# Performance work log

Hardware: AMD Instinct MI355X
Metric: run time of the kernel (lower is better)

The kernel has to match this reference:

```python
import jax, jax.numpy as jnp
import numpy as np

# graph / model constants (match init_kwargs and input_specs)
B, NPG, EPG, ML = 4, 10000, 32000, 128      # graphs, nodes/graph, edges/graph, latent
I_LAYERS, K_ITERS, J_HEADS = 3, 4, 6         # GNN layers, outer iters (n_iter+r_iter), I*n_iter
N, E, E2 = B * NPG, B * EPG, EPG // 2
ZETA = 1e-6
P_EXP = 1.852                                # Hazen-Williams exponent


def setup_inputs() -> dict:
    rng = np.random.default_rng(0)
    sndr_l, rcvr_l, r_l = [], [], []
    for b in range(B):
        off = b * NPG
        s = rng.integers(0, NPG, E2)
        t = rng.integers(0, NPG, E2)
        # per graph: first half forward edges, second half reversed (directionality trick)
        sndr_l.append(np.concatenate([s, t]) + off)
        rcvr_l.append(np.concatenate([t, s]) + off)
        rr = rng.uniform(0.1, 1.0, (E2, 1)).astype(np.float32)
        r_l.append(np.concatenate([rr, rr], 0))
    sndr = jnp.asarray(np.concatenate(sndr_l), dtype=jnp.int32)
    rcvr = jnp.asarray(np.concatenate(rcvr_l), dtype=jnp.int32)
    r = jnp.asarray(np.concatenate(r_l, 0))
    res = rng.random(N) < 0.01
    res[np.arange(B) * NPG] = True  # at least one reservoir per graph
    h_star = np.where(res, rng.uniform(50.0, 100.0, N), 0.0).astype(np.float32)
    d_star = rng.uniform(0.0, 0.1, N).astype(np.float32)
    x = jnp.asarray(np.stack([h_star, d_star], 1))
    ks = jax.random.split(jax.random.key(0), 9)
    def w(k, shape):
        return jax.random.normal(k, shape, jnp.float32) / np.sqrt(shape[-2])
    return dict(
        x=x, r=r,
        W_node_in=w(ks[0], (2, ML)), W_edge_in=w(ks[1], (2, ML)),
        Wf1=w(ks[2], (3 * ML, ML)), Wf2=w(ks[3], (ML, ML)), Wf3=w(ks[4], (ML, 1)),
        We1=w(ks[5], (I_LAYERS, 3 * ML, ML)), We2=w(ks[6], (I_LAYERS, ML, ML)),
        Wn1=w(ks[7], (I_LAYERS, 2 * ML, ML)), Wn2=w(ks[8], (I_LAYERS, ML, ML)),
        sndr=sndr, rcvr=rcvr)


def _compute_net_flows(h, r, sndr, rcvr):
    # invert Hazen-Williams: dh = r * sign(q) * |q|^1.852  =>  q = sign(dh)*(|dh|/r)^(1/1.852)
    dh = h[sndr] - h[rcvr]
    q = jnp.sign(dh) * ((jnp.abs(dh) + ZETA) / (r + ZETA)) ** (1.0 / P_EXP)
    d = jax.ops.segment_sum(q[:, 0], rcvr, num_segments=N)[:, None]
    return d, q


def _construct_heads(h_star, q, r, sndr, rcvr):
    # physics-informed head reconstruction: propagate heads from reservoirs along edges
    res = h_star != 0
    hl = r * jnp.sign(q) * jnp.abs(q) ** P_EXP  # head loss per edge
    h = h_star
    for _ in range(J_HEADS):
        cand = (h[sndr] - hl)[:, 0]
        agg = jax.ops.segment_max(cand, rcvr, num_segments=N)[:, None]
        agg = jnp.where(agg > -1e30, agg, h)  # nodes with no incoming edge keep value
        h = jnp.where(res, h_star, jnp.maximum(h, agg))
    return h


def _forward(x, r, W_node_in, W_edge_in, Wf1, Wf2, Wf3, We1, We2, Wn1, Wn2, sndr, rcvr):
    selu = jax.nn.selu
    h_star, d_star = x[:, 0:1], x[:, 1:2]
    d_hat, q_hat = _compute_net_flows(h_star, r, sndr, rcvr)
    q_tilde = q_hat
    h_tilde = h_star
    for _ in range(K_ITERS):
        # f_1: embed node/edge features
        g = selu(jnp.concatenate([d_hat, d_star], -1)) @ W_node_in    # [N, ML]
        z = selu(jnp.concatenate([q_tilde, q_hat], -1)) @ W_edge_in   # [E, ML]
        for i in range(I_LAYERS):
            # edge update MLP on (g_sndr, g_rcvr, z), then max-aggregate to nodes
            m = selu(jnp.concatenate([g[sndr], g[rcvr], z], -1))       # [E, 3ML]
            z = selu(m @ We1[i]) @ We2[i]
            agg = jax.ops.segment_max(z, rcvr, num_segments=N)
            agg = jnp.where(agg > -1e30, agg, 0.0)
            g = selu(selu(jnp.concatenate([g, agg], -1)) @ Wn1[i]) @ Wn2[i]
        # MLP lambda: flow residual
        lam_in = selu(jnp.concatenate([g[sndr], g[rcvr], z], -1))
        q_hat = q_hat + selu(selu(lam_in @ Wf1) @ Wf2) @ Wf3
        # enforce antisymmetric directionality: q(rev) = -q(fwd)
        q_in = q_hat.reshape(B, EPG, 1)[:, :E2]
        q_hat = jnp.concatenate([q_in, -q_in], axis=1).reshape(E, 1)
        # demand reconstruction (eq. 3): scatter-add flows into receivers
        d_hat = jax.ops.segment_sum(q_hat[:, 0], rcvr, num_segments=N)[:, None]
        # f_2: physics-informed head reconstruction + net flows (eq. 6-8)
        h_tilde = _construct_heads(h_star, q_hat, r, sndr, rcvr)
        d_tilde, q_tilde = _compute_net_flows(h_tilde, r, sndr, rcvr)
    return h_tilde


def reference(x, r, W_node_in, W_edge_in, Wf1, Wf2, Wf3, We1, We2, Wn1, Wn2, sndr, rcvr):
    return _forward(x, r, W_node_in, W_edge_in, Wf1, Wf2, Wf3, We1, We2, Wn1, Wn2, sndr, rcvr)
```

## Files before the change

### kernel.cpp

```cpp
#include <hip/hip_runtime.h>
#include <hip/hip_bf16.h>
#include <math.h>

#define NPGc  10000
#define EPGc  32000
#define MLc   128
#define NNc   40000
#define NEc   128000
#define E2c   16000
#define ZETAc 1e-6f
#define INVPc 0.53995680345572354f
#define PEXPc 1.852f
#define NSB   ((NNc + 255) / 256)

typedef __attribute__((ext_vector_type(8))) short short8;
typedef __attribute__((ext_vector_type(4))) float f32x4;

__device__ __forceinline__ float selu_f(float x) {
    float e = __expf(x) - 1.0f;
    return 1.0507009873554805f * (x > 0.0f ? x : 1.6732632423543772f * e);
}
__device__ __forceinline__ void splitt(float v, unsigned& hi, unsigned& lo) {
    unsigned u = __float_as_uint(v);
    hi = u >> 16;
    float rem = v - __uint_as_float(u & 0xffff0000u);
    __hip_bfloat16 l = __float2bfloat16(rem);
    lo = (unsigned short)*reinterpret_cast<short*>(&l);
}
__device__ __forceinline__ short bf16_rne(float v) {
    __hip_bfloat16 h = __float2bfloat16(v);
    return *reinterpret_cast<short*>(&h);
}
__device__ __forceinline__ float signf(float x) {
    return (x > 0.0f) ? 1.0f : (x < 0.0f ? -1.0f : 0.0f);
}
__device__ __forceinline__ int rfl(int v) { return __builtin_amdgcn_readfirstlane(v); }

__device__ __forceinline__ void load_lds16(const void* src, void* dst) {
    __builtin_amdgcn_global_load_lds(
        (const __attribute__((address_space(1))) unsigned*)src,
        (__attribute__((address_space(3))) unsigned*)dst, 16, 0, 0);
}

#define WCA (8 * 12 * 64)
#define WCB (8 * 4 * 64)
#define WCC (8 * 8 * 64)
#define WCTOT (3 * (WCA + WCB + WCC + WCB) + WCA + WCB)

__global__ void k_wconv_all(
    const float* __restrict__ We1, const float* __restrict__ We2,
    const float* __restrict__ Wn1, const float* __restrict__ Wn2,
    const float* __restrict__ Wf1, const float* __restrict__ Wf2,
    short* __restrict__ we1h, short* __restrict__ we2h,
    short* __restrict__ wn1h, short* __restrict__ wn2h,
    short* __restrict__ wf1h, short* __restrict__ wf2h) {
    int gid = blockIdx.x * 256 + threadIdx.x;
    if (gid >= WCTOT) return;
    const float* src; short* dst; int nkc; int lg;
    if (gid < 3 * WCA) {
        int L = gid / WCA; lg = gid - L * WCA;
        src = We1 + (size_t)L * 384 * 128; dst = we1h + (size_t)L * 128 * 384; nkc = 12;
    } else if (gid < 3 * WCA + 3 * WCB) {
        int g2 = gid - 3 * WCA; int L = g2 / WCB; lg = g2 - L * WCB;
        src = We2 + (size_t)L * 128 * 128; dst = we2h + (size_t)L * 128 * 128; nkc = 4;
    } else if (gid < 3 * WCA + 3 * WCB + 3 * WCC) {
        int g2 = gid - 3 * WCA - 3 * WCB; int L = g2 / WCC; lg = g2 - L * WCC;
        src = Wn1 + (size_t)L * 256 * 128; dst = wn1h + (size_t)L * 128 * 256; nkc = 8;
    } else if (gid < 3 * WCA + 3 * WCB + 3 * WCC + 3 * WCB) {
        int g2 = gid - 3 * WCA - 3 * WCB - 3 * WCC; int L = g2 / WCB; lg = g2 - L * WCB;
        src = Wn2 + (size_t)L * 128 * 128; dst = wn2h + (size_t)L * 128 * 128; nkc = 4;
    } else if (gid < 3 * WCA + 3 * WCB + 3 * WCC + 3 * WCB + WCA) {
        lg = gid - (3 * WCA + 3 * WCB + 3 * WCC + 3 * WCB);
        src = Wf1; dst = wf1h; nkc = 12;
    } else {
        lg = gid - (3 * WCA + 3 * WCB + 3 * WCC + 3 * WCB + WCA);
        src = Wf2; dst = wf2h; nkc = 4;
    }
    int lane = lg & 63;
    int frag = lg >> 6;
    int kc = frag % nkc;
    int ct = frag / nkc;
    int col = ct * 16 + (lane & 15);
    int kbase = kc * 32 + (lane >> 4) * 8;
    size_t o = (size_t)lg * 8;
#pragma unroll
    for (int j = 0; j < 8; j++)
        dst[o + j] = bf16_rne(src[(size_t)(kbase + j) * 128 + col]);
}

__global__ void k_zero_i(int* p, int n) {
    int i = blockIdx.x * 256 + threadIdx.x;
    if (i < n) p[i] = 0;
}
__global__ void k_count(const int* __restrict__ rcvr, int* __restrict__ deg) {
    int e = blockIdx.x * 256 + threadIdx.x;
    if (e < NEc) atomicAdd(&deg[rcvr[e]], 1);
}
__global__ void k_scan1(const int* __restrict__ deg, int* __restrict__ partial) {
    __shared__ int buf[256];
    int t = threadIdx.x;
    int i = blockIdx.x * 256 + t;
    buf[t] = (i < NNc) ? deg[i] : 0;
    __syncthreads();
    for (int off = 128; off > 0; off >>= 1) {
        if (t < off) buf[t] += buf[t + off];
        __syncthreads();
    }
    if (t == 0) partial[blockIdx.x] = buf[0];
}
__global__ void k_scan2(int* __restrict__ partial) {
    __shared__ int buf[256];
    int t = threadIdx.x;
    int v = (t < NSB) ? partial[t] : 0;
    buf[t] = v;
    __syncthreads();
    for (int off = 1; off < 256; off <<= 1) {
        int u = (t >= off) ? buf[t - off] : 0;
        __syncthreads();
        buf[t] += u;
        __syncthreads();
    }
    if (t < NSB) partial[t] = buf[t] - v;
}
__global__ void k_scan3(const int* __restrict__ deg, const int* __restrict__ partial,
                        int* __restrict__ rowstart, int* __restrict__ cursor) {
    __shared__ int buf[256];
    int t = threadIdx.x;
    int i = blockIdx.x * 256 + t;
    int v = (i < NNc) ? deg[i] : 0;
    buf[t] = v;
    __syncthreads();
    for (int off = 1; off < 256; off <<= 1) {
        int u = (t >= off) ? buf[t - off] : 0;
        __syncthreads();
        buf[t] += u;
        __syncthreads();
    }
    int excl = partial[blockIdx.x] + buf[t] - v;
    if (i < NNc) { rowstart[i] = excl; cursor[i] = excl; }
    if (i == NNc - 1) rowstart[NNc] = excl + v;
}
__global__ void k_scatter(const int* __restrict__ sndr, const int* __restrict__ rcvr,
                          int* __restrict__ cursor, int2* __restrict__ csr_se) {
    int e = blockIdx.x * 256 + threadIdx.x;
    if (e >= NEc) return;
    int rv = rcvr[e];
    int p = atomicAdd(&cursor[rv], 1);
    csr_se[p] = make_int2(sndr[e], e);
}

__global__ void k_qinit(const float* __restrict__ x, const float* __restrict__ r,
                        const int* __restrict__ sndr, const int* __restrict__ rcvr,
                        float* __restrict__ qh, float* __restrict__ qt) {
    int e = blockIdx.x * 256 + threadIdx.x;
    if (e >= NEc) return;
    float hv = x[2 * sndr[e]] - x[2 * rcvr[e]];
    float q = signf(hv) * __powf((fabsf(hv) + ZETAc) / (r[e] + ZETAc), INVPc);
    qh[e] = q; qt[e] = q;
}
__global__ void k_flows_q(const float* __restrict__ h, const float* __restrict__ r,
                          const int* __restrict__ sndr, const int* __restrict__ rcvr,
                          float* __restrict__ qt) {
    int e = blockIdx.x * 256 + threadIdx.x;
    if (e >= NEc) return;
    float hv = h[sndr[e]] - h[rcvr[e]];
    qt[e] = signf(hv) * __powf((fabsf(hv) + ZETAc) / (r[e] + ZETAc), INVPc);
}

__global__ __launch_bounds__(256) void k_node_in_f(
    const float* __restrict__ qh, const int* __restrict__ rowstart,
    const int2* __restrict__ csr_se, const float* __restrict__ x,
    const float* __restrict__ W ,
    unsigned* __restrict__ gh_u, unsigned* __restrict__ gl_u) {
    const int tid = threadIdx.x;
    const int lane = tid & 63;
    const int n = rfl(blockIdx.x * 4 + (tid >> 6));
    if (n >= NNc) return;
    int p0 = rfl(rowstart[n]), p1 = rfl(rowstart[n + 1]);
    float s = 0.0f;
    for (int p = p0 + lane; p < p1; p += 64) s += qh[csr_se[p].y];
#pragma unroll
    for (int off = 1; off < 64; off <<= 1) s += __shfl_xor(s, off, 64);
    float s0 = selu_f(s);
    float s1 = selu_f(x[2 * n + 1]);
    int c = lane * 2;
    float g0 = s0 * W[c]     + s1 * W[MLc + c];
    float g1 = s0 * W[c + 1] + s1 * W[MLc + c + 1];
    unsigned h0, l0, h1, l1;
    splitt(selu_f(g0), h0, l0);
    splitt(selu_f(g1), h1, l1);
    gh_u[(size_t)n * 64 + lane] = h0 | (h1 << 16);
    gl_u[(size_t)n * 64 + lane] = l0 | (l1 << 16);
}

__global__ __launch_bounds__(256) void k_head_iter(
    const float* __restrict__ x, const float* __restrict__ hin, int hstride,
    const float* __restrict__ hl, const int* __restrict__ rowstart,
    const int2* __restrict__ csr_se, float* __restrict__ hout) {
    int t = blockIdx.x * 256 + threadIdx.x;
    int n = t >> 2;
    int sub = t & 3;
    if (n >= NNc) return;
    float hv = hin[(size_t)n * hstride];
    float m = -3.0e38f;
    int p0 = rowstart[n], p1 = rowstart[n + 1];
    for (int p = p0 + sub; p < p1; p += 4) {
        int2 se = csr_se[p];
        m = fmaxf(m, hin[(size_t)se.x * hstride] - hl[se.y]);
    }
    m = fmaxf(m, __shfl_xor(m, 1, 64));
    m = fmaxf(m, __shfl_xor(m, 2, 64));
    if (sub == 0) {
        float a = (m > -1e30f) ? m : hv;
        float hstar = x[2 * n];
        hout[n] = (hstar != 0.0f) ? hstar : fmaxf(hv, a);
    }
}


__global__ __launch_bounds__(512) void k_edge_mlp_mfma(
    const unsigned* __restrict__ gh_u, const unsigned* __restrict__ gl_u,
    const unsigned* __restrict__ zh_u, const unsigned* __restrict__ zl_u,
    short* __restrict__ zoh_s, short* __restrict__ zol_s,
    const short* __restrict__ W1h, const short* __restrict__ W2h,
    const int* __restrict__ sndr, const int* __restrict__ rcvr,
    const float* __restrict__ qt, const float* __restrict__ qh,
    const float* __restrict__ Wei, int zmode) {
    __shared__ short smem[12288];
    const int tid = threadIdx.x;
    const int bi = blockIdx.x;
    const int x7 = bi & 7, jj = bi >> 3;
    const int e0 = ((x7 >> 1) * 1000 + (x7 & 1) * 500 + jj) * 32;
    const int lane = tid & 63, wave = tid >> 6;
    const int l15 = lane & 15, quad = lane >> 4;

    const int plane = wave & 1;
    const int srt = (wave >> 1) & 1;
    const int kc0 = wave >> 2;
    const int erow = e0 + srt * 16 + l15;
    const size_t bs = (size_t)sndr[erow] * 64 + quad * 4;
    const size_t br = (size_t)rcvr[erow] * 64 + quad * 4;
    const size_t bz = (size_t)erow * 64 + quad * 4;
    const unsigned* pg = plane ? gl_u : gh_u;
    const unsigned* pz = plane ? zl_u : zh_u;
    short* dbase = smem + plane * 6144 + srt * 512;
    const int nkc = zmode ? 8 : 12;

    short8 zvh, zvl;
    const int kzi = wave >> 1, rtz = wave & 1;
    if (zmode) {
        const int e = e0 + rtz * 16 + l15;
        const float sqt = selu_f(qt[e]), sqh = selu_f(qh[e]);
#pragma unroll
        for (int j = 0; j < 8; j++) {
            int c = kzi * 32 + quad * 8 + j;
            float z = sqt * Wei[c] + sqh * Wei[MLc + c];
            unsigned h, l;
            splitt(selu_f(z), h, l);
            zvh[j] = (short)h; zvl[j] = (short)l;
        }
    }

#pragma unroll
    for (int u = 0; u < 3; u++) {
        int kc = kc0 + 2 * u;
        int region = kc >> 2, kcl = kc & 3;
        const unsigned* src = (region == 0) ? (pg + bs + kcl * 16)
                                            : (pg + br + kcl * 16);
        load_lds16(src, dbase + kc * 1024);
    }
    __syncthreads();

    const int ct = wave;
    const int col = ct * 16 + l15;
    const short* abase = smem + lane * 8;

    f32x4 acc[2];
    acc[0] = (f32x4){0.f, 0.f, 0.f, 0.f};
    acc[1] = (f32x4){0.f, 0.f, 0.f, 0.f};
    __builtin_amdgcn_s_setprio(1);
#pragma unroll
    for (int kc = 0; kc < 6; kc++) {
        size_t wo = ((size_t)(ct * 12 + kc) * 64 + lane) * 8;
        short8 bh = *(const short8*)&W1h[wo];
#pragma unroll
        for (int rt = 0; rt < 2; rt++) {
            const short* ap = abase + (kc * 2 + rt) * 512;
            short8 ah = *(const short8*)ap;
            short8 al = *(const short8*)(ap + 6144);
            acc[rt] = __builtin_amdgcn_mfma_f32_16x16x32_bf16(ah, bh, acc[rt], 0, 0, 0);
            acc[rt] = __builtin_amdgcn_mfma_f32_16x16x32_bf16(al, bh, acc[rt], 0, 0, 0);
        }
    }
    __builtin_amdgcn_s_setprio(0);
    __syncthreads();

#pragma unroll
    for (int u = 0; u < 3; u++) {
        int kc = 6 + kc0 + 2 * u;
        if (kc < nkc) {
            int region = kc >> 2, kcl = kc & 3;
            const unsigned* src = (region == 1) ? (pg + br + kcl * 16)
                                                : (pz + bz + kcl * 16);
            load_lds16(src, dbase + (kc - 6) * 1024);
        }
    }
    if (zmode) {
        int slot = (2 + kzi) * 2 + rtz;
        *(short8*)&smem[slot * 512 + lane * 8] = zvh;
        *(short8*)&smem[6144 + slot * 512 + lane * 8] = zvl;
    }
    __syncthreads();

    __builtin_amdgcn_s_setprio(1);
#pragma unroll
    for (int kc6 = 0; kc6 < 6; kc6++) {
        int kc = 6 + kc6;
        size_t wo = ((size_t)(ct * 12 + kc) * 64 + lane) * 8;
        short8 bh = *(const short8*)&W1h[wo];
#pragma unroll
        for (int rt = 0; rt < 2; rt++) {
            const short* ap = abase + (kc6 * 2 + rt) * 512;
            short8 ah = *(const short8*)ap;
            short8 al = *(const short8*)(ap + 6144);
            acc[rt] = __builtin_amdgcn_mfma_f32_16x16x32_bf16(ah, bh, acc[rt], 0, 0, 0);
            acc[rt] = __builtin_amdgcn_mfma_f32_16x16x32_bf16(al, bh, acc[rt], 0, 0, 0);
        }
    }
    __builtin_amdgcn_s_setprio(0);
    __syncthreads();

    {
        const int kc2 = ct >> 1;
        const int q2 = ((ct & 1) << 1) | (l15 >> 3);
        const int jj2 = l15 & 7;
#pragma unroll
        for (int rt = 0; rt < 2; rt++) {
#pragma unroll
            for (int rr = 0; rr < 4; rr++) {
                unsigned h, l;
                splitt(selu_f(acc[rt][rr]), h, l);
                int o = (kc2 * 2 + rt) * 512 + (q2 * 16 + quad * 4 + rr) * 8 + jj2;
                smem[o] = (short)h;
                smem[4096 + o] = (short)l;
            }
        }
    }
    __syncthreads();

    f32x4 acc2[2];
    acc2[0] = (f32x4){0.f, 0.f, 0.f, 0.f};
    acc2[1] = (f32x4){0.f, 0.f, 0.f, 0.f};
    __builtin_amdgcn_s_setprio(1);
#pragma unroll
    for (int kc = 0; kc < 4; kc++) {
        size_t wo = ((size_t)(ct * 4 + kc) * 64 + lane) * 8;
        short8 bh = *(const short8*)&W2h[wo];
#pragma unroll
        for (int rt = 0; rt < 2; rt++) {
            const short* ap = abase + (kc * 2 + rt) * 512;
            short8 ah = *(const short8*)ap;
            short8 al = *(const short8*)(ap + 4096);
            acc2[rt] = __builtin_amdgcn_mfma_f32_16x16x32_bf16(ah, bh, acc2[rt], 0, 0, 0);
            acc2[rt] = __builtin_amdgcn_mfma_f32_16x16x32_bf16(al, bh, acc2[rt], 0, 0, 0);
        }
    }
    __builtin_amdgcn_s_setprio(0);
#pragma unroll
    for (int rt = 0; rt < 2; rt++) {
#pragma unroll
        for (int rr = 0; rr < 4; rr++) {
            unsigned h, l;
            splitt(selu_f(acc2[rt][rr]), h, l);
            size_t o = (size_t)(e0 + rt * 16 + quad * 4 + rr) * 128 + col;
            zoh_s[o] = (short)h;
            zol_s[o] = (short)l;
        }
    }
}

__global__ __launch_bounds__(512) void k_node_mlp_mfma(
    const unsigned* __restrict__ gh_u, const unsigned* __restrict__ gl_u,
    short* __restrict__ goh_s, short* __restrict__ gol_s,
    const unsigned* __restrict__ zh_u, const unsigned* __restrict__ zl_u,
    const int* __restrict__ rowstart, const int2* __restrict__ csr_se,
    const short* __restrict__ W1h, const short* __restrict__ W2h) {
    __shared__ short smem[16384];
    const int tid = threadIdx.x;
    const int n0 = blockIdx.x * 32;
    const int lane = tid & 63, wave = tid >> 6;
    const int l15 = lane & 15, quad = lane >> 4;

    {
        const int plane = wave & 1;
        const int rt = (wave >> 1) & 1;
        const int kc0 = wave >> 2;
        const size_t bg = (size_t)(n0 + rt * 16 + l15) * 64 + quad * 4;
        const unsigned* pg = plane ? gl_u : gh_u;
        short* dbase = smem + plane * 8192 + rt * 512;
#pragma unroll
        for (int u = 0; u < 2; u++) {
            int kc = kc0 + 2 * u;
            load_lds16(pg + bg + kc * 16, dbase + kc * 1024);
        }
    }
    for (int idx = tid; idx < 32 * 64; idx += 512) {
        int row = rfl(idx >> 6);
        int cp = idx & 63;
        int n = rfl(n0 + row);
        int p0 = rfl(rowstart[n]), p1 = rfl(rowstart[n + 1]);
        float b0 = -3.0e38f, b1 = -3.0e38f;
        unsigned bh0 = 0, bl0 = 0, bh1 = 0, bl1 = 0;
        for (int p = p0; p < p1; p++) {
            int ey = rfl(csr_se[p].y);
            size_t o = (size_t)ey * 64 + cp;
            unsigned vh = zh_u[o], vl = zl_u[o];
            float f0 = __uint_as_float(vh << 16) + __uint_as_float(vl << 16);
            float f1 = __uint_as_float(vh & 0xffff0000u) + __uint_as_float(vl & 0xffff0000u);
            if (f0 > b0) { b0 = f0; bh0 = vh & 0xffffu; bl0 = vl & 0xffffu; }
            if (f1 > b1) { b1 = f1; bh1 = vh & 0xffff0000u; bl1 = vl & 0xffff0000u; }
        }
        int rt = row >> 4;
        int kc = 4 + (cp >> 4);
        int o2 = (kc * 2 + rt) * 512 + (((cp >> 2) & 3) * 16 + (row & 15)) * 8 + 2 * (cp & 3);
        *(unsigned*)&smem[o2] = bh0 | bh1;
        *(unsigned*)&smem[8192 + o2] = bl0 | bl1;
    }
    __syncthreads();

    const int ct = wave;
    const int col = ct * 16 + l15;
    const short* abase = smem + lane * 8;

    f32x4 acc[2];
    acc[0] = (f32x4){0.f, 0.f, 0.f, 0.f};
    acc[1] = (f32x4){0.f, 0.f, 0.f, 0.f};
    __builtin_amdgcn_s_setprio(1);
#pragma unroll
    for (int kc = 0; kc < 8; kc++) {
        size_t wo = ((size_t)(ct * 8 + kc) * 64 + lane) * 8;
        short8 bh = *(const short8*)&W1h[wo];
#pragma unroll
        for (int rt = 0; rt < 2; rt++) {
            const short* ap = abase + (kc * 2 + rt) * 512;
            short8 ah = *(const short8*)ap;
            short8 al = *(const short8*)(ap + 8192);
            acc[rt] = __builtin_amdgcn_mfma_f32_16x16x32_bf16(ah, bh, acc[rt], 0, 0, 0);
            acc[rt] = __builtin_amdgcn_mfma_f32_16x16x32_bf16(al, bh, acc[rt], 0, 0, 0);
        }
    }
    __builtin_amdgcn_s_setprio(0);
    __syncthreads();
    {
        const int kc2 = ct >> 1;
        const int q2 = ((ct & 1) << 1) | (l15 >> 3);
        const int jj2 = l15 & 7;
#pragma unroll
        for (int rt = 0; rt < 2; rt++) {
#pragma unroll
            for (int rr = 0; rr < 4; rr++) {
                unsigned h, l;
                splitt(selu_f(acc[rt][rr]), h, l);
                int o = (kc2 * 2 + rt) * 512 + (q2 * 16 + quad * 4 + rr) * 8 + jj2;
                smem[o] = (short)h;
                smem[4096 + o] = (short)l;
            }
        }
    }
    __syncthreads();

    f32x4 acc2[2];
    acc2[0] = (f32x4){0.f, 0.f, 0.f, 0.f};
    acc2[1] = (f32x4){0.f, 0.f, 0.f, 0.f};
    __builtin_amdgcn_s_setprio(1);
#pragma unroll
    for (int kc = 0; kc < 4; kc++) {
        size_t wo = ((size_t)(ct * 4 + kc) * 64 + lane) * 8;
        short8 bh = *(const short8*)&W2h[wo];
#pragma unroll
        for (int rt = 0; rt < 2; rt++) {
            const short* ap = abase + (kc * 2 + rt) * 512;
            short8 ah = *(const short8*)ap;
            short8 al = *(const short8*)(ap + 4096);
            acc2[rt] = __builtin_amdgcn_mfma_f32_16x16x32_bf16(ah, bh, acc2[rt], 0, 0, 0);
            acc2[rt] = __builtin_amdgcn_mfma_f32_16x16x32_bf16(al, bh, acc2[rt], 0, 0, 0);
        }
    }
    __builtin_amdgcn_s_setprio(0);
#pragma unroll
    for (int rt = 0; rt < 2; rt++) {
#pragma unroll
        for (int rr = 0; rr < 4; rr++) {
            unsigned h, l;
            splitt(selu_f(acc2[rt][rr]), h, l);
            size_t o = (size_t)(n0 + rt * 16 + quad * 4 + rr) * 128 + col;
            goh_s[o] = (short)h;
            gol_s[o] = (short)l;
        }
    }
}

__global__ __launch_bounds__(512) void k_wf_mfma(
    const unsigned* __restrict__ gh_u, const unsigned* __restrict__ gl_u,
    const unsigned* __restrict__ zh_u, const unsigned* __restrict__ zl_u,
    const short* __restrict__ W1h, const short* __restrict__ W2h,
    const float* __restrict__ W3 ,
    const int* __restrict__ sndr, const int* __restrict__ rcvr,
    const float* __restrict__ r,
    float* __restrict__ qh, float* __restrict__ hl) {
    __shared__ short smem[12288];
    __shared__ float red[32 * 8];
    const int tid = threadIdx.x;
    const int bi = blockIdx.x;
    const int x7 = bi & 7, jj = bi >> 3;
    const int fi0 = ((x7 >> 1) * 500 + (x7 & 1) * 250 + jj) * 32;
    const int b = fi0 / E2c;
    const int ebase = b * EPGc - b * E2c;
    const int lane = tid & 63, wave = tid >> 6;
    const int l15 = lane & 15, quad = lane >> 4;

    const int plane = wave & 1;
    const int srt = (wave >> 1) & 1;
    const int kc0 = wave >> 2;
    const int erow = ebase + fi0 + srt * 16 + l15;
    const size_t bs = (size_t)sndr[erow] * 64 + quad * 4;
    const size_t br = (size_t)rcvr[erow] * 64 + quad * 4;
    const size_t bz = (size_t)erow * 64 + quad * 4;
    const unsigned* pg = plane ? gl_u : gh_u;
    const unsigned* pz = plane ? zl_u : zh_u;
    short* dbase = smem + plane * 6144 + srt * 512;

#pragma unroll
    for (int u = 0; u < 3; u++) {
        int kc = kc0 + 2 * u;
        int region = kc >> 2, kcl = kc & 3;
        const unsigned* src = (region == 0) ? (pg + bs + kcl * 16)
                                            : (pg + br + kcl * 16);
        load_lds16(src, dbase + kc * 1024);
    }
    __syncthreads();

    const int ct = wave;
    const int col = ct * 16 + l15;
    const short* abase = smem + lane * 8;

    f32x4 acc[2];
    acc[0] = (f32x4){0.f, 0.f, 0.f, 0.f};
    acc[1] = (f32x4){0.f, 0.f, 0.f, 0.f};
    __builtin_amdgcn_s_setprio(1);
#pragma unroll
    for (int kc = 0; kc < 6; kc++) {
        size_t wo = ((size_t)(ct * 12 + kc) * 64 + lane) * 8;
        short8 bh = *(const short8*)&W1h[wo];
#pragma unroll
        for (int rt = 0; rt < 2; rt++) {
            const short* ap = abase + (kc * 2 + rt) * 512;
            short8 ah = *(const short8*)ap;
            short8 al = *(const short8*)(ap + 6144);
            acc[rt] = __builtin_amdgcn_mfma_f32_16x16x32_bf16(ah, bh, acc[rt], 0, 0, 0);
            acc[rt] = __builtin_amdgcn_mfma_f32_16x16x32_bf16(al, bh, acc[rt], 0, 0, 0);
        }
    }
    __builtin_amdgcn_s_setprio(0);
    __syncthreads();

#pragma unroll
    for (int u = 0; u < 3; u++) {
        int kc = 6 + kc0 + 2 * u;
        int region = kc >> 2, kcl = kc & 3;
        const unsigned* src = (region == 1) ? (pg + br + kcl * 16)
                                            : (pz + bz + kcl * 16);
        load_lds16(src, dbase + (kc - 6) * 1024);
    }
    __syncthreads();

    __builtin_amdgcn_s_setprio(1);
#pragma unroll
    for (int kc6 = 0; kc6 < 6; kc6++) {
        int kc = 6 + kc6;
        size_t wo = ((size_t)(ct * 12 + kc) * 64 + lane) * 8;
        short8 bh = *(const short8*)&W1h[wo];
#pragma unroll
        for (int rt = 0; rt < 2; rt++) {
            const short* ap = abase + (kc6 * 2 + rt) * 512;
            short8 ah = *(const short8*)ap;
            short8 al = *(const short8*)(ap + 6144);
            acc[rt] = __builtin_amdgcn_mfma_f32_16x16x32_bf16(ah, bh, acc[rt], 0, 0, 0);
            acc[rt] = __builtin_amdgcn_mfma_f32_16x16x32_bf16(al, bh, acc[rt], 0, 0, 0);
        }
    }
    __builtin_amdgcn_s_setprio(0);
    __syncthreads();

    {
        const int kc2 = ct >> 1;
        const int q2 = ((ct & 1) << 1) | (l15 >> 3);
        const int jj2 = l15 & 7;
#pragma unroll
        for (int rt = 0; rt < 2; rt++) {
#pragma unroll
            for (int rr = 0; rr < 4; rr++) {
                unsigned h, l;
                splitt(selu_f(acc[rt][rr]), h, l);
                int o = (kc2 * 2 + rt) * 512 + (q2 * 16 + quad * 4 + rr) * 8 + jj2;
                smem[o] = (short)h;
                smem[4096 + o] = (short)l;
            }
        }
    }
    __syncthreads();

    f32x4 acc2[2];
    acc2[0] = (f32x4){0.f, 0.f, 0.f, 0.f};
    acc2[1] = (f32x4){0.f, 0.f, 0.f, 0.f};
    __builtin_amdgcn_s_setprio(1);
#pragma unroll
    for (int kc = 0; kc < 4; kc++) {
        size_t wo = ((size_t)(ct * 4 + kc) * 64 + lane) * 8;
        short8 bh = *(const short8*)&W2h[wo];
#pragma unroll
        for (int rt = 0; rt < 2; rt++) {
            const short* ap = abase + (kc * 2 + rt) * 512;
            short8 ah = *(const short8*)ap;
            short8 al = *(const short8*)(ap + 4096);
            acc2[rt] = __builtin_amdgcn_mfma_f32_16x16x32_bf16(ah, bh, acc2[rt], 0, 0, 0);
            acc2[rt] = __builtin_amdgcn_mfma_f32_16x16x32_bf16(al, bh, acc2[rt], 0, 0, 0);
        }
    }
    __builtin_amdgcn_s_setprio(0);
    float w3 = W3[col];
    float p[8];
#pragma unroll
    for (int rt = 0; rt < 2; rt++)
#pragma unroll
        for (int rr = 0; rr < 4; rr++) p[rt * 4 + rr] = selu_f(acc2[rt][rr]) * w3;
#pragma unroll
    for (int off = 1; off < 16; off <<= 1) {
#pragma unroll
        for (int i = 0; i < 8; i++) p[i] += __shfl_xor(p[i], off, 64);
    }
    if (l15 == 0) {
#pragma unroll
        for (int rt = 0; rt < 2; rt++)
#pragma unroll
            for (int rr = 0; rr < 4; rr++)
                red[(rt * 16 + quad * 4 + rr) * 8 + ct] = p[rt * 4 + rr];
    }
    __syncthreads();
    if (tid < 32) {
        float f = 0.0f;
#pragma unroll
        for (int c = 0; c < 8; c++) f += red[tid * 8 + c];
        int e = ebase + fi0 + tid;
        float qn = qh[e] + f;
        qh[e] = qn;
        qh[e + E2c] = -qn;
        float hv = r[e] * signf(qn) * __powf(fabsf(qn), PEXPc);
        hl[e] = hv;
        hl[e + E2c] = -hv;
    }
}


extern "C" void kernel_launch(void* const* d_in, const int* in_sizes, int n_in,
                              void* d_out, int out_size, void* d_ws, size_t ws_size,
                              hipStream_t stream) {
    const float* x   = (const float*)d_in[0];
    const float* r   = (const float*)d_in[1];
    const float* Wni = (const float*)d_in[2];
    const float* Wei = (const float*)d_in[3];
    const float* Wf1 = (const float*)d_in[4];
    const float* Wf2 = (const float*)d_in[5];
    const float* Wf3 = (const float*)d_in[6];
    const float* We1 = (const float*)d_in[7];
    const float* We2 = (const float*)d_in[8];
    const float* Wn1 = (const float*)d_in[9];
    const float* Wn2 = (const float*)d_in[10];
    const int* sndr  = (const int*)d_in[11];
    const int* rcvr  = (const int*)d_in[12];
    float* out = (float*)d_out;

    char* wp = (char*)d_ws;
    auto carve = [&](size_t bytes) -> void* {
        void* ret = (void*)wp;
        wp += (bytes + 255) & ~(size_t)255;
        return ret;
    };
    unsigned* gh_u = (unsigned*)carve((size_t)NNc * 64 * 4);
    unsigned* gl_u = (unsigned*)carve((size_t)NNc * 64 * 4);
    unsigned* zAh  = (unsigned*)carve((size_t)NEc * 64 * 4);
    unsigned* zAl  = (unsigned*)carve((size_t)NEc * 64 * 4);
    unsigned* zBh  = (unsigned*)carve((size_t)NEc * 64 * 4);
    unsigned* zBl  = (unsigned*)carve((size_t)NEc * 64 * 4);
    float* qh     = (float*)carve((size_t)NEc * 4);
    float* qt     = (float*)carve((size_t)NEc * 4);
    float* hl     = (float*)carve((size_t)NEc * 4);
    float* hA     = (float*)carve((size_t)NNc * 4);
    float* hB     = (float*)carve((size_t)NNc * 4);
    int*   deg    = (int*)carve((size_t)NNc * 4);
    int*   cursor = (int*)carve((size_t)NNc * 4);
    int*   rowst  = (int*)carve((size_t)(NNc + 1) * 4);
    int*   part   = (int*)carve((size_t)NSB * 4);
    int2*  csr_se = (int2*)carve((size_t)NEc * 8);
    short* we1h   = (short*)carve((size_t)3 * 128 * 384 * 2);
    short* we2h   = (short*)carve((size_t)3 * 128 * 128 * 2);
    short* wn1h   = (short*)carve((size_t)3 * 128 * 256 * 2);
    short* wn2h   = (short*)carve((size_t)3 * 128 * 128 * 2);
    short* wf1h   = (short*)carve((size_t)128 * 384 * 2);
    short* wf2h   = (short*)carve((size_t)128 * 128 * 2);

    const int TB = 256;
    const int gN  = (NNc + TB - 1) / TB;
    const int gE  = (NEc + TB - 1) / TB;

    k_wconv_all<<<(WCTOT + TB - 1) / TB, TB, 0, stream>>>(
        We1, We2, Wn1, Wn2, Wf1, Wf2, we1h, we2h, wn1h, wn2h, wf1h, wf2h);

    k_zero_i<<<gN, TB, 0, stream>>>(deg, NNc);
    k_count<<<gE, TB, 0, stream>>>(rcvr, deg);
    k_scan1<<<NSB, TB, 0, stream>>>(deg, part);
    k_scan2<<<1, TB, 0, stream>>>(part);
    k_scan3<<<NSB, TB, 0, stream>>>(deg, part, rowst, cursor);
    k_scatter<<<gE, TB, 0, stream>>>(sndr, rcvr, cursor, csr_se);

    k_qinit<<<gE, TB, 0, stream>>>(x, r, sndr, rcvr, qh, qt);

    const int gH = (NNc * 4 + 255) / 256;
    for (int kit = 0; kit < 4; kit++) {
        k_node_in_f<<<(NNc + 3) / 4, TB, 0, stream>>>(qh, rowst, csr_se, x, Wni, gh_u, gl_u);
        unsigned *zin_h = zAh, *zin_l = zAl, *zout_h = zAh, *zout_l = zAl;
        for (int i = 0; i < 3; i++) {
            zin_h = zout_h; zin_l = zout_l;
            zout_h = (i & 1) ? zAh : zBh;
            zout_l = (i & 1) ? zAl : zBl;
            k_edge_mlp_mfma<<<NEc / 32, 512, 0, stream>>>(
                gh_u, gl_u, zin_h, zin_l, (short*)zout_h, (short*)zout_l,
                we1h + (size_t)i * 128 * 384,
                we2h + (size_t)i * 128 * 128,
                sndr, rcvr, qt, qh, Wei, (i == 0) ? 1 : 0);
            k_node_mlp_mfma<<<NNc / 32, 512, 0, stream>>>(
                gh_u, gl_u, (short*)gh_u, (short*)gl_u, zout_h, zout_l, rowst, csr_se,
                wn1h + (size_t)i * 128 * 256,
                wn2h + (size_t)i * 128 * 128);
        }
        k_wf_mfma<<<(4 * E2c) / 32, 512, 0, stream>>>(
            gh_u, gl_u, zout_h, zout_l, wf1h, wf2h, Wf3, sndr, rcvr,
            r, qh, hl);
        const float* hin = x; int hstride = 2;
        float* cur = hA;
        for (int jh = 0; jh < 6; jh++) {
            float* dst = (jh == 5) ? ((kit == 3) ? out : hB) : cur;
            k_head_iter<<<gH, TB, 0, stream>>>(x, hin, hstride, hl, rowst, csr_se, dst);
            hin = dst; hstride = 1;
            cur = (dst == hA) ? hB : hA;
        }
        if (kit < 3) k_flows_q<<<gE, TB, 0, stream>>>(hB, r, sndr, rcvr, qt);
    }
}
```

Before: 1.389 ms.

## Fuse head iterations and flow update into one cooperative kernel with grid sync

Replaces the six per-iteration head-propagation launches and the separate flow-recompute launch with a single cooperative kernel that uses grid-wide syncs between steps. This removes roughly six launches per outer iteration and keeps row bounds and h_star in registers across steps. In exchange, every step now pays a grid barrier, and the cooperative launch needs all 625 blocks to be resident at once.

```diff
diff --git a/kernel.cpp b/kernel.cpp
--- a/kernel.cpp
+++ b/kernel.cpp
@@ -1,6 +1,9 @@
 #include <hip/hip_runtime.h>
+#include <hip/hip_cooperative_groups.h>
 #include <hip/hip_bf16.h>
 #include <math.h>
+
+namespace cg = cooperative_groups;
 
 #define NPGc  10000
 #define EPGc  32000
@@ -158,14 +161,6 @@
     float q = signf(hv) * __powf((fabsf(hv) + ZETAc) / (r[e] + ZETAc), INVPc);
     qh[e] = q; qt[e] = q;
 }
-__global__ void k_flows_q(const float* __restrict__ h, const float* __restrict__ r,
-                          const int* __restrict__ sndr, const int* __restrict__ rcvr,
-                          float* __restrict__ qt) {
-    int e = blockIdx.x * 256 + threadIdx.x;
-    if (e >= NEc) return;
-    float hv = h[sndr[e]] - h[rcvr[e]];
-    qt[e] = signf(hv) * __powf((fabsf(hv) + ZETAc) / (r[e] + ZETAc), INVPc);
-}
 
 __global__ __launch_bounds__(256) void k_node_in_f(
     const float* __restrict__ qh, const int* __restrict__ rowstart,
@@ -193,27 +188,58 @@
     gl_u[(size_t)n * 64 + lane] = l0 | (l1 << 16);
 }
 
-__global__ __launch_bounds__(256) void k_head_iter(
-    const float* __restrict__ x, const float* __restrict__ hin, int hstride,
-    const float* __restrict__ hl, const int* __restrict__ rowstart,
-    const int2* __restrict__ csr_se, float* __restrict__ hout) {
-    int t = blockIdx.x * 256 + threadIdx.x;
-    int n = t >> 2;
-    int sub = t & 3;
-    if (n >= NNc) return;
-    float hv = hin[(size_t)n * hstride];
-    float m = -3.0e38f;
-    int p0 = rowstart[n], p1 = rowstart[n + 1];
-    for (int p = p0 + sub; p < p1; p += 4) {
-        int2 se = csr_se[p];
-        m = fmaxf(m, hin[(size_t)se.x * hstride] - hl[se.y]);
-    }
-    m = fmaxf(m, __shfl_xor(m, 1, 64));
-    m = fmaxf(m, __shfl_xor(m, 2, 64));
-    if (sub == 0) {
-        float a = (m > -1e30f) ? m : hv;
-        float hstar = x[2 * n];
-        hout[n] = (hstar != 0.0f) ? hstar : fmaxf(hv, a);
+#define HGRID ((NNc * 4 + 255) / 256)
+
+__global__ __launch_bounds__(256) void k_head_all(
+    const float* __restrict__ x, const float* __restrict__ hl,
+    const int* __restrict__ rowstart, const int2* __restrict__ csr_se,
+    float* __restrict__ hA, float* __restrict__ hB, float* __restrict__ dst5,
+    const int* __restrict__ sndr, const int* __restrict__ rcvr,
+    const float* __restrict__ r, float* __restrict__ qt, int do_flows) {
+    cg::grid_group grid = cg::this_grid();
+    const int t = blockIdx.x * 256 + threadIdx.x;
+    const int n = t >> 2;
+    const int sub = t & 3;
+    const bool act = (n < NNc);
+    int p0 = 0, p1 = 0;
+    float hstar = 0.0f;
+    if (act) {
+        p0 = rowstart[n]; p1 = rowstart[n + 1];
+        hstar = x[2 * n];
+    }
+
+#define HEAD_STEP(HIN, HSTRIDE, DST) do {                                     \
+        if (act) {                                                            \
+            const float* hin_ = (HIN);                                        \
+            float hv = hin_[(size_t)n * (HSTRIDE)];                           \
+            float m = -3.0e38f;                                               \
+            for (int p = p0 + sub; p < p1; p += 4) {                          \
+                int2 se = csr_se[p];                                          \
+                m = fmaxf(m, hin_[(size_t)se.x * (HSTRIDE)] - hl[se.y]);      \
+            }                                                                 \
+            m = fmaxf(m, __shfl_xor(m, 1, 64));                               \
+            m = fmaxf(m, __shfl_xor(m, 2, 64));                               \
+            if (sub == 0) {                                                   \
+                float a = (m > -1e30f) ? m : hv;                              \
+                (DST)[n] = (hstar != 0.0f) ? hstar : fmaxf(hv, a);            \
+            }                                                                 \
+        }                                                                     \
+        grid.sync();                                                          \
+    } while (0)
+
+    HEAD_STEP(x,  2, hA);
+    HEAD_STEP(hA, 1, hB);
+    HEAD_STEP(hB, 1, hA);
+    HEAD_STEP(hA, 1, hB);
+    HEAD_STEP(hB, 1, hA);
+    HEAD_STEP(hA, 1, dst5);
+#undef HEAD_STEP
+
+    if (do_flows) {
+        for (int e = t; e < NEc; e += HGRID * 256) {
+            float hv = dst5[sndr[e]] - dst5[rcvr[e]];
+            qt[e] = signf(hv) * __powf((fabsf(hv) + ZETAc) / (r[e] + ZETAc), INVPc);
+        }
     }
 }
 
@@ -725,7 +751,6 @@
 
     k_qinit<<<gE, TB, 0, stream>>>(x, r, sndr, rcvr, qh, qt);
 
-    const int gH = (NNc * 4 + 255) / 256;
     for (int kit = 0; kit < 4; kit++) {
         k_node_in_f<<<(NNc + 3) / 4, TB, 0, stream>>>(qh, rowst, csr_se, x, Wni, gh_u, gl_u);
         unsigned *zin_h = zAh, *zin_l = zAl, *zout_h = zAh, *zout_l = zAl;
@@ -746,14 +771,20 @@
         k_wf_mfma<<<(4 * E2c) / 32, 512, 0, stream>>>(
             gh_u, gl_u, zout_h, zout_l, wf1h, wf2h, Wf3, sndr, rcvr,
             r, qh, hl);
-        const float* hin = x; int hstride = 2;
-        float* cur = hA;
-        for (int jh = 0; jh < 6; jh++) {
-            float* dst = (jh == 5) ? ((kit == 3) ? out : hB) : cur;
-            k_head_iter<<<gH, TB, 0, stream>>>(x, hin, hstride, hl, rowst, csr_se, dst);
-            hin = dst; hstride = 1;
-            cur = (dst == hA) ? hB : hA;
-        }
-        if (kit < 3) k_flows_q<<<gE, TB, 0, stream>>>(hB, r, sndr, rcvr, qt);
-    }
-}
+        {
+            float* dst5 = (kit == 3) ? out : hB;
+            int do_flows = (kit < 3) ? 1 : 0;
+            const float* xa = x; const float* hla = hl;
+            const int* rsa = rowst; const int2* csa = csr_se;
+            float* hAa = hA; float* hBa = hB;
+            const int* sna = sndr; const int* rca = rcvr;
+            const float* ra = r; float* qta = qt;
+            void* args[] = { (void*)&xa, (void*)&hla, (void*)&rsa, (void*)&csa,
+                             (void*)&hAa, (void*)&hBa, (void*)&dst5,
+                             (void*)&sna, (void*)&rca, (void*)&ra, (void*)&qta,
+                             (void*)&do_flows };
+            hipLaunchCooperativeKernel((void*)k_head_all, dim3(HGRID), dim3(256),
+                                       args, 0, stream);
+        }
+    }
+}
```

New measurement: 3.205 ms. 2.31x slower.
